# Kernel tuning notes

Hardware: AMD Instinct MI355X
Metric: run time of the kernel (lower is better)

## Reference

```python
import jax, jax.numpy as jnp
import numpy as np

EPS = 1e-5

def _act_quant(x):
    # per-token int8 absmax quantization with STE passthrough
    s = 127.0 / jnp.clip(jnp.max(jnp.abs(x), axis=-1, keepdims=True), EPS, None)
    xq = jnp.clip(jnp.round(x * s), -128.0, 127.0) / s
    return x + jax.lax.stop_gradient(xq - x)

def _weight_quant(w):
    # ternary {-1,0,1} abs-mean quantization with STE passthrough
    s = 1.0 / jnp.clip(jnp.mean(jnp.abs(w)), EPS, None)
    wq = jnp.clip(jnp.round(w * s), -1.0, 1.0) / s
    return w + jax.lax.stop_gradient(wq - w)

def bitlinear(x, w, b=None):
    y = _act_quant(x) @ _weight_quant(w).T
    return y if b is None else y + b

def setup_inputs() -> dict:
    key = jax.random.key(0)
    ks = jax.random.split(key, 6)
    B, T, C = 64, 256, 1024
    std = 1.0 / np.sqrt(C)
    return {
        "x": jax.random.normal(ks[0], (B, T, C), dtype=jnp.float32),
        "Wq": jax.random.normal(ks[1], (C, C), dtype=jnp.float32) * std,
        "Wk": jax.random.normal(ks[2], (C, C), dtype=jnp.float32) * std,
        "Wv": jax.random.normal(ks[3], (C, C), dtype=jnp.float32) * std,
        "Wp": jax.random.normal(ks[4], (C, C), dtype=jnp.float32) * std,
        "bp": jnp.zeros((C,), dtype=jnp.float32),
        "n_head": 16,
    }

def reference(x, Wq, Wk, Wv, Wp, bp, n_head):
    B, T, C = x.shape
    hd = C // n_head
    def heads(t):  # [B,T,C] -> [B,H,T,hd]
        return t.reshape(B, T, n_head, hd).transpose(0, 2, 1, 3)
    q = heads(bitlinear(x, Wq))
    k = heads(bitlinear(x, Wk))
    v = heads(bitlinear(x, Wv))
    attn = jnp.einsum("bhqd,bhkd->bhqk", q, k) * (1.0 / np.sqrt(hd))
    causal = jnp.tril(jnp.ones((T, T), dtype=bool))
    attn = jnp.where(causal, attn, -jnp.inf)
    attn = jax.nn.softmax(attn, axis=-1)
    y = jnp.einsum("bhqk,bhkd->bhqd", attn, v)
    y = y.transpose(0, 2, 1, 3).reshape(B, T, C)
    return bitlinear(y, Wp, bp)
```

## Files before the change

### kernel.cpp

```cpp
#include <hip/hip_runtime.h>
#include <math.h>

#define AS1 __attribute__((address_space(1)))
#define AS3 __attribute__((address_space(3)))

typedef unsigned short u16;
typedef signed char i8;
typedef short bf16x8 __attribute__((ext_vector_type(8)));
typedef float f32x4 __attribute__((ext_vector_type(4)));
typedef int i32x4 __attribute__((ext_vector_type(4)));

static constexpr int BB = 64, T = 256, C = 1024, H = 16, HD = 64;
static constexpr int M = BB * T;
static constexpr float EPSF = 1e-5f;

static constexpr size_t W8_OFF   = 0;
static constexpr size_t XQ8_OFF  = 4ull  << 20;
static constexpr size_t RSX_OFF  = 20ull << 20;
static constexpr size_t RSY_OFF  = (20ull << 20) + (64 << 10);
static constexpr size_t WSUM_OFF = (20ull << 20) + (128 << 10);
static constexpr size_t WPART_OFF= WSUM_OFF + 64;
static constexpr size_t QB_OFF   = 21ull << 20;
static constexpr size_t KB_OFF   = 53ull << 20;
static constexpr size_t VT_OFF   = 85ull << 20;

__device__ __forceinline__ u16 f2bf_rne(float f) {
    unsigned x = __float_as_uint(f);
    unsigned r = x + 0x7FFF + ((x >> 16) & 1);
    return (u16)(r >> 16);
}

__global__ __launch_bounds__(256) void wsum1_kernel(const float* __restrict__ Wq,
    const float* __restrict__ Wk, const float* __restrict__ Wv,
    const float* __restrict__ Wp, double* __restrict__ wpart)
{
    const int mat = blockIdx.x >> 6;
    const float* W = (mat == 0) ? Wq : (mat == 1) ? Wk : (mat == 2) ? Wv : Wp;
    const int t = threadIdx.x;
    const int base = (blockIdx.x & 63) * 256 + t;
    double s = 0.0;
    for (int i = 0; i < 64; ++i) s += (double)fabsf(W[base + (i << 14)]);
    #pragma unroll
    for (int off = 32; off >= 1; off >>= 1) s += __shfl_down(s, off);
    __shared__ double red[4];
    if ((t & 63) == 0) red[t >> 6] = s;
    __syncthreads();
    if (t == 0) wpart[blockIdx.x] = red[0] + red[1] + red[2] + red[3];
}

__global__ __launch_bounds__(256) void wsum2_kernel(const double* __restrict__ wpart,
                                                    double* __restrict__ wsum)
{
    const int t = threadIdx.x;
    double s = wpart[t];
    #pragma unroll
    for (int off = 32; off >= 1; off >>= 1) s += __shfl_down(s, off);
    if ((t & 63) == 0) wsum[t >> 6] = s;
}

__global__ __launch_bounds__(256) void wquant_kernel(const float* __restrict__ Wq,
    const float* __restrict__ Wk, const float* __restrict__ Wv,
    const float* __restrict__ Wp, const double* __restrict__ wsum,
    i8* __restrict__ w8)
{
    const int mat = blockIdx.x >> 10;
    const float* W = (mat == 0) ? Wq : (mat == 1) ? Wk : (mat == 2) ? Wv : Wp;
    const float mean = (float)(wsum[mat] * (1.0 / 1048576.0));
    const float s = 1.0f / fmaxf(mean, EPSF);
    const int idx = (blockIdx.x & 1023) * 256 + threadIdx.x;
    float4 w = ((const float4*)W)[idx];
    char4 o;
    o.x = (i8)(int)fminf(fmaxf(rintf(w.x * s), -1.f), 1.f);
    o.y = (i8)(int)fminf(fmaxf(rintf(w.y * s), -1.f), 1.f);
    o.z = (i8)(int)fminf(fmaxf(rintf(w.z * s), -1.f), 1.f);
    o.w = (i8)(int)fminf(fmaxf(rintf(w.w * s), -1.f), 1.f);
    ((char4*)(w8 + (size_t)mat * 1048576))[idx] = o;
}

__global__ __launch_bounds__(256) void actquant_kernel(const float* __restrict__ x,
    i8* __restrict__ xq, float* __restrict__ rs)
{
    const int row = blockIdx.x;
    const int t = threadIdx.x;
    float4 v = ((const float4*)(x + (size_t)row * C))[t];
    float m = fmaxf(fmaxf(fabsf(v.x), fabsf(v.y)), fmaxf(fabsf(v.z), fabsf(v.w)));
    #pragma unroll
    for (int off = 32; off >= 1; off >>= 1) m = fmaxf(m, __shfl_down(m, off));
    __shared__ float red[4];
    if ((t & 63) == 0) red[t >> 6] = m;
    __syncthreads();
    float mm = fmaxf(fmaxf(red[0], red[1]), fmaxf(red[2], red[3]));
    mm = fmaxf(mm, EPSF);
    const float s = 127.0f / mm;
    if (t == 0) rs[row] = mm / 127.0f;
    char4 o;
    o.x = (i8)(int)fminf(fmaxf(rintf(v.x * s), -128.f), 127.f);
    o.y = (i8)(int)fminf(fmaxf(rintf(v.y * s), -128.f), 127.f);
    o.z = (i8)(int)fminf(fmaxf(rintf(v.z * s), -128.f), 127.f);
    o.w = (i8)(int)fminf(fmaxf(rintf(v.w * s), -128.f), 127.f);
    ((char4*)(xq + (size_t)row * C))[t] = o;
}

template<bool QKV, int NNB>
__global__ __launch_bounds__(512, 2) void gemm_kernel(const i8* __restrict__ A,
    const i8* __restrict__ w8, const float* __restrict__ rs_row,
    const double* __restrict__ wsum, u16* __restrict__ qb, u16* __restrict__ kb,
    u16* __restrict__ vt, float* __restrict__ outp, const float* __restrict__ bias)
{
    constexpr int K = 1024, N = 1024;
    constexpr int NT = 16;
    __shared__ __align__(16) i8 Asm[4][256 * 64];
    __shared__ __align__(16) i8 Bsm[4][256 * 64];

    const int t = threadIdx.x;

    const int nwg = NNB * 64;
    const int wg = (int)blockIdx.x;
    const int swz = (wg & 7) * (nwg >> 3) + (wg >> 3);
    const int mb = swz / NNB, nb = swz % NNB;
    const int m0 = mb * 256;
    const int mat = QKV ? (nb >> 2) : 3;
    const int n0m = QKV ? ((nb & 3) * 256) : (nb * 256);
    const i8* Bw = w8 + (size_t)mat * 1048576;

    const int lane = t & 63, wv = t >> 6;
    const int wm = wv >> 2, wn = wv & 3;
    const int mr = lane & 15, quad = lane >> 4;

    const int g1 = t, g2 = t + 512;
    const int L1 = (g1 * 16) ^ (((g1 >> 3) & 7) << 4);
    const int L2 = (g2 * 16) ^ (((g2 >> 3) & 7) << 4);
    const i8* a1 = A  + (size_t)(m0  + (L1 >> 6)) * K + (L1 & 63);
    const i8* a2 = A  + (size_t)(m0  + (L2 >> 6)) * K + (L2 & 63);
    const i8* b1 = Bw + (size_t)(n0m + (L1 >> 6)) * K + (L1 & 63);
    const i8* b2 = Bw + (size_t)(n0m + (L2 >> 6)) * K + (L2 & 63);

    const int vvs = (mr >> 1) & 7;
    int aoff[8], boff[4];
    #pragma unroll
    for (int m = 0; m < 8; ++m)
        aoff[m] = ((wm * 128 + m * 16 + mr) * 64 + quad * 16) ^ (vvs << 4);
    #pragma unroll
    for (int n = 0; n < 4; ++n)
        boff[n] = ((wn * 64 + n * 16 + mr) * 64 + quad * 16) ^ (vvs << 4);

    i32x4 acc[8][4];
    #pragma unroll
    for (int m = 0; m < 8; ++m)
        #pragma unroll
        for (int n = 0; n < 4; ++n) acc[m][n] = (i32x4){0, 0, 0, 0};

    #pragma unroll
    for (int p = 0; p < 2; ++p) {
        const int k0 = p * 64;
        __builtin_amdgcn_global_load_lds((const AS1 void*)(a1 + k0), (AS3 void*)&Asm[p][g1 * 16], 16, 0, 0);
        __builtin_amdgcn_global_load_lds((const AS1 void*)(a2 + k0), (AS3 void*)&Asm[p][g2 * 16], 16, 0, 0);
        __builtin_amdgcn_global_load_lds((const AS1 void*)(b1 + k0), (AS3 void*)&Bsm[p][g1 * 16], 16, 0, 0);
        __builtin_amdgcn_global_load_lds((const AS1 void*)(b2 + k0), (AS3 void*)&Bsm[p][g2 * 16], 16, 0, 0);
    }
    asm volatile("s_waitcnt vmcnt(4)" ::: "memory");
    __builtin_amdgcn_s_barrier();

    for (int tt = 0; tt < NT; ++tt) {
        const i8* Ac = Asm[tt & 3];
        const i8* Bc = Bsm[tt & 3];
        i8* An = Asm[(tt + 2) & 3];
        i8* Bn = Bsm[(tt + 2) & 3];
        const int kn = (tt + 2) * 64;
        const bool pf = (tt < NT - 2);

        if (pf) {
            __builtin_amdgcn_global_load_lds((const AS1 void*)(a1 + kn), (AS3 void*)&An[g1 * 16], 16, 0, 0);
            __builtin_amdgcn_global_load_lds((const AS1 void*)(a2 + kn), (AS3 void*)&An[g2 * 16], 16, 0, 0);
        }
        i32x4 af[8];
        #pragma unroll
        for (int m = 0; m < 8; ++m) af[m] = *(const i32x4*)&Ac[aoff[m]];
        i32x4 bf0 = *(const i32x4*)&Bc[boff[0]];
        i32x4 bf1 = *(const i32x4*)&Bc[boff[1]];
        __builtin_amdgcn_s_barrier();
        asm volatile("s_waitcnt lgkmcnt(0)" ::: "memory");
        __builtin_amdgcn_s_setprio(1);
        #pragma unroll
        for (int m = 0; m < 8; ++m) {
            acc[m][0] = __builtin_amdgcn_mfma_i32_16x16x64_i8(af[m], bf0, acc[m][0], 0, 0, 0);
            acc[m][1] = __builtin_amdgcn_mfma_i32_16x16x64_i8(af[m], bf1, acc[m][1], 0, 0, 0);
        }
        __builtin_amdgcn_s_setprio(0);
        __builtin_amdgcn_s_barrier();

        if (pf) {
            __builtin_amdgcn_global_load_lds((const AS1 void*)(b1 + kn), (AS3 void*)&Bn[g1 * 16], 16, 0, 0);
            __builtin_amdgcn_global_load_lds((const AS1 void*)(b2 + kn), (AS3 void*)&Bn[g2 * 16], 16, 0, 0);
        }
        i32x4 bf2 = *(const i32x4*)&Bc[boff[2]];
        i32x4 bf3 = *(const i32x4*)&Bc[boff[3]];
        __builtin_amdgcn_s_barrier();
        asm volatile("s_waitcnt lgkmcnt(0)" ::: "memory");
        __builtin_amdgcn_s_setprio(1);
        #pragma unroll
        for (int m = 0; m < 8; ++m) {
            acc[m][2] = __builtin_amdgcn_mfma_i32_16x16x64_i8(af[m], bf2, acc[m][2], 0, 0, 0);
            acc[m][3] = __builtin_amdgcn_mfma_i32_16x16x64_i8(af[m], bf3, acc[m][3], 0, 0, 0);
        }
        __builtin_amdgcn_s_setprio(0);
        if (tt < NT - 2) {
            asm volatile("s_waitcnt vmcnt(4)" ::: "memory");
        } else if (tt < NT - 1) {
            asm volatile("s_waitcnt vmcnt(0)" ::: "memory");
        }
        __builtin_amdgcn_s_barrier();
    }

    float wsc = fmaxf((float)(wsum[mat] * (1.0 / 1048576.0)), EPSF);
    if (QKV && mat == 0) wsc *= 0.125f;

    if (QKV && mat == 2) {
        #pragma unroll
        for (int m = 0; m < 8; ++m) {
            const int gr0 = m0 + wm * 128 + m * 16 + quad * 4;
            const int bbi = gr0 >> 8, tl = gr0 & 255;
            const float4 rs4 = *(const float4*)(rs_row + gr0);
            #pragma unroll
            for (int n = 0; n < 4; ++n) {
                const int gcol = n0m + wn * 64 + n * 16 + mr;
                ushort4 o;
                o.x = f2bf_rne((float)acc[m][n][0] * rs4.x * wsc);
                o.y = f2bf_rne((float)acc[m][n][1] * rs4.y * wsc);
                o.z = f2bf_rne((float)acc[m][n][2] * rs4.z * wsc);
                o.w = f2bf_rne((float)acc[m][n][3] * rs4.w * wsc);
                *(ushort4*)(vt + (size_t)(bbi * 1024 + gcol) * 256 + tl) = o;
            }
        }
        return;
    }

    u16* ob = QKV ? ((mat == 0) ? qb : kb) : nullptr;
    #pragma unroll
    for (int m = 0; m < 8; ++m) {
        const int gr0 = m0 + wm * 128 + m * 16 + quad * 4;
        #pragma unroll
        for (int r = 0; r < 4; ++r) {
            const int grow = gr0 + r;
            const float sc = rs_row[grow] * wsc;
            #pragma unroll
            for (int n = 0; n < 4; ++n) {
                const int gcol = n0m + wn * 64 + n * 16 + mr;
                const float val = (float)acc[m][n][r] * sc;
                if (QKV) {
                    ob[(size_t)grow * N + gcol] = f2bf_rne(val);
                } else {
                    outp[(size_t)grow * N + gcol] = val + bias[gcol];
                }
            }
        }
    }
}

__global__ __launch_bounds__(256) void attn_kernel(const u16* __restrict__ qb,
    const u16* __restrict__ kb, const u16* __restrict__ vt, float* __restrict__ y)
{
    const int t = threadIdx.x;
    const int qt = 3 - (int)(blockIdx.x >> 10);
    const int bh = blockIdx.x & 1023;
    const int b = bh >> 4, h = bh & 15;
    const int w = t >> 6, lane = t & 63;
    const int cl = lane & 15, quad = lane >> 4;
    const size_t gb = (size_t)(b * T) * 1024 + h * 64;
    const u16* vtb = vt + (size_t)(b * 1024 + h * 64) * 256;

    const int qrow = qt * 64 + w * 16;
    const int jtiles = (qrow >> 4) + 1;

    const u16* qrp = qb + gb + (size_t)(qrow + cl) * 1024 + quad * 8;
    bf16x8 qf0 = *(const bf16x8*)qrp;
    bf16x8 qf1 = *(const bf16x8*)(qrp + 32);

    f32x4 Sp[16];
    #pragma unroll
    for (int i = 0; i < 16; ++i) Sp[i] = (f32x4){0.f, 0.f, 0.f, 0.f};

    const u16* krp = kb + gb + (size_t)cl * 1024 + quad * 8;
    #pragma unroll
    for (int jt = 0; jt < 16; ++jt) {
        if (jt < jtiles) {
            const u16* kp = krp + (size_t)(jt * 16) * 1024;
            bf16x8 kf0 = *(const bf16x8*)kp;
            bf16x8 kf1 = *(const bf16x8*)(kp + 32);
            Sp[jt] = __builtin_amdgcn_mfma_f32_16x16x32_bf16(kf0, qf0, Sp[jt], 0, 0, 0);
            Sp[jt] = __builtin_amdgcn_mfma_f32_16x16x32_bf16(kf1, qf1, Sp[jt], 0, 0, 0);
            if (jt == jtiles - 1) {
                #pragma unroll
                for (int r = 0; r < 4; ++r)
                    if (quad * 4 + r > cl) Sp[jt][r] = -INFINITY;
            }
        }
    }

    float mx = -INFINITY;
    #pragma unroll
    for (int jt = 0; jt < 16; ++jt) if (jt < jtiles) {
        #pragma unroll
        for (int r = 0; r < 4; ++r) mx = fmaxf(mx, Sp[jt][r]);
    }
    mx = fmaxf(mx, __shfl_xor(mx, 16));
    mx = fmaxf(mx, __shfl_xor(mx, 32));
    float l = 0.f;
    #pragma unroll
    for (int jt = 0; jt < 16; ++jt) if (jt < jtiles) {
        #pragma unroll
        for (int r = 0; r < 4; ++r) {
            float p = __expf(Sp[jt][r] - mx);
            Sp[jt][r] = p;
            l += p;
        }
    }
    l += __shfl_xor(l, 16);
    l += __shfl_xor(l, 32);

    f32x4 O[4];
    #pragma unroll
    for (int i = 0; i < 4; ++i) O[i] = (f32x4){0.f, 0.f, 0.f, 0.f};

    const int s01 = ((quad & 1) << 5) + cl;
    const bool lo = quad < 2;
    #pragma unroll
    for (int jc = 0; jc < 8; ++jc) {
        if (jc * 2 < jtiles) {
            int pk[2][2];
            #pragma unroll
            for (int s = 0; s < 2; ++s) {
                const f32x4 v = Sp[jc * 2 + s];
                pk[s][0] = (int)((unsigned)f2bf_rne(v[0]) | ((unsigned)f2bf_rne(v[1]) << 16));
                pk[s][1] = (int)((unsigned)f2bf_rne(v[2]) | ((unsigned)f2bf_rne(v[3]) << 16));
            }
            int a0 = __shfl(pk[0][0], s01),      a1 = __shfl(pk[0][1], s01);
            int a2 = __shfl(pk[0][0], s01 + 16), a3 = __shfl(pk[0][1], s01 + 16);
            int b0 = __shfl(pk[1][0], s01),      b1 = __shfl(pk[1][1], s01);
            int b2 = __shfl(pk[1][0], s01 + 16), b3 = __shfl(pk[1][1], s01 + 16);
            union { int i[4]; bf16x8 v; } af;
            af.i[0] = lo ? a0 : b0;
            af.i[1] = lo ? a1 : b1;
            af.i[2] = lo ? a2 : b2;
            af.i[3] = lo ? a3 : b3;
            const u16* vp = vtb + (size_t)cl * 256 + jc * 32 + quad * 8;
            #pragma unroll
            for (int dt = 0; dt < 4; ++dt) {
                bf16x8 vf = *(const bf16x8*)(vp + (size_t)dt * 16 * 256);
                O[dt] = __builtin_amdgcn_mfma_f32_16x16x32_bf16(af.v, vf, O[dt], 0, 0, 0);
            }
        }
    }

    float inv[4];
    #pragma unroll
    for (int r = 0; r < 4; ++r) inv[r] = 1.0f / __shfl(l, quad * 4 + r);
    #pragma unroll
    for (int dt = 0; dt < 4; ++dt)
        #pragma unroll
        for (int r = 0; r < 4; ++r)
            y[gb + (size_t)(qrow + quad * 4 + r) * 1024 + dt * 16 + cl] = O[dt][r] * inv[r];
}

extern "C" void kernel_launch(void* const* d_in, const int* in_sizes, int n_in,
                              void* d_out, int out_size, void* d_ws, size_t ws_size,
                              hipStream_t stream) {
    (void)in_sizes; (void)n_in; (void)out_size; (void)ws_size;
    const float* x  = (const float*)d_in[0];
    const float* Wq = (const float*)d_in[1];
    const float* Wk = (const float*)d_in[2];
    const float* Wv = (const float*)d_in[3];
    const float* Wp = (const float*)d_in[4];
    const float* bp = (const float*)d_in[5];
    float* out = (float*)d_out;
    char* ws = (char*)d_ws;

    i8*     w8   = (i8*)(ws + W8_OFF);
    i8*     xq8  = (i8*)(ws + XQ8_OFF);
    float*  rsx  = (float*)(ws + RSX_OFF);
    float*  rsy  = (float*)(ws + RSY_OFF);
    double* wsum = (double*)(ws + WSUM_OFF);
    double* wpart= (double*)(ws + WPART_OFF);
    u16*    qb   = (u16*)(ws + QB_OFF);
    u16*    kb   = (u16*)(ws + KB_OFF);
    u16*    vt   = (u16*)(ws + VT_OFF);

    wsum1_kernel<<<256, 256, 0, stream>>>(Wq, Wk, Wv, Wp, wpart);
    wsum2_kernel<<<1, 256, 0, stream>>>(wpart, wsum);
    wquant_kernel<<<4096, 256, 0, stream>>>(Wq, Wk, Wv, Wp, wsum, w8);
    actquant_kernel<<<M, 256, 0, stream>>>(x, xq8, rsx);

    gemm_kernel<true, 12><<<768, 512, 0, stream>>>(xq8, w8, rsx, wsum, qb, kb, vt, nullptr, nullptr);

    attn_kernel<<<4 * 1024, 256, 0, stream>>>(qb, kb, vt, out);

    actquant_kernel<<<M, 256, 0, stream>>>(out, xq8, rsy);
    gemm_kernel<false, 4><<<256, 512, 0, stream>>>(xq8, w8, rsy, wsum, nullptr, nullptr, nullptr, out, bp);
}
```

Measured before the change: 322.0 us.

## Merge GEMM main-loop halves into single barrier phase; remap attention block order

The int8 GEMM main loop now issues all four prefetch loads at the top of each iteration and loads every A and B fragment at once. It then runs all 32 MFMAs in one burst, so three of the four barriers and explicit lgkmcnt waits per k-step are gone, and sched_barrier fences keep the compiler from moving code across the loop boundary. The attention kernel gets a launch-bounds occupancy hint of 8 blocks and a new blockIdx mapping that interleaves the four query tiles of each group of 8 (batch,head) pairs, aiming for better K/V cache locality and load balance. Removing the mid-iteration barrier relies on the four-buffer ring and the remaining waits still keeping the LDS hazards safe. Holding all fragments live at once also raises register pressure.

```diff
diff --git a/kernel.cpp b/kernel.cpp
--- a/kernel.cpp
+++ b/kernel.cpp
@@ -160,6 +160,7 @@
     }
     asm volatile("s_waitcnt vmcnt(4)" ::: "memory");
     __builtin_amdgcn_s_barrier();
+    __builtin_amdgcn_sched_barrier(0);
 
     for (int tt = 0; tt < NT; ++tt) {
         const i8* Ac = Asm[tt & 3];
@@ -167,49 +168,35 @@
         i8* An = Asm[(tt + 2) & 3];
         i8* Bn = Bsm[(tt + 2) & 3];
         const int kn = (tt + 2) * 64;
-        const bool pf = (tt < NT - 2);
-
-        if (pf) {
+
+        if (tt < NT - 2) {
             __builtin_amdgcn_global_load_lds((const AS1 void*)(a1 + kn), (AS3 void*)&An[g1 * 16], 16, 0, 0);
             __builtin_amdgcn_global_load_lds((const AS1 void*)(a2 + kn), (AS3 void*)&An[g2 * 16], 16, 0, 0);
-        }
-        i32x4 af[8];
-        #pragma unroll
-        for (int m = 0; m < 8; ++m) af[m] = *(const i32x4*)&Ac[aoff[m]];
-        i32x4 bf0 = *(const i32x4*)&Bc[boff[0]];
-        i32x4 bf1 = *(const i32x4*)&Bc[boff[1]];
-        __builtin_amdgcn_s_barrier();
-        asm volatile("s_waitcnt lgkmcnt(0)" ::: "memory");
-        __builtin_amdgcn_s_setprio(1);
-        #pragma unroll
-        for (int m = 0; m < 8; ++m) {
-            acc[m][0] = __builtin_amdgcn_mfma_i32_16x16x64_i8(af[m], bf0, acc[m][0], 0, 0, 0);
-            acc[m][1] = __builtin_amdgcn_mfma_i32_16x16x64_i8(af[m], bf1, acc[m][1], 0, 0, 0);
-        }
-        __builtin_amdgcn_s_setprio(0);
-        __builtin_amdgcn_s_barrier();
-
-        if (pf) {
             __builtin_amdgcn_global_load_lds((const AS1 void*)(b1 + kn), (AS3 void*)&Bn[g1 * 16], 16, 0, 0);
             __builtin_amdgcn_global_load_lds((const AS1 void*)(b2 + kn), (AS3 void*)&Bn[g2 * 16], 16, 0, 0);
         }
-        i32x4 bf2 = *(const i32x4*)&Bc[boff[2]];
-        i32x4 bf3 = *(const i32x4*)&Bc[boff[3]];
-        __builtin_amdgcn_s_barrier();
-        asm volatile("s_waitcnt lgkmcnt(0)" ::: "memory");
+
+        i32x4 af[8], bf[4];
+        #pragma unroll
+        for (int m = 0; m < 8; ++m) af[m] = *(const i32x4*)&Ac[aoff[m]];
+        #pragma unroll
+        for (int n = 0; n < 4; ++n) bf[n] = *(const i32x4*)&Bc[boff[n]];
+
         __builtin_amdgcn_s_setprio(1);
         #pragma unroll
-        for (int m = 0; m < 8; ++m) {
-            acc[m][2] = __builtin_amdgcn_mfma_i32_16x16x64_i8(af[m], bf2, acc[m][2], 0, 0, 0);
-            acc[m][3] = __builtin_amdgcn_mfma_i32_16x16x64_i8(af[m], bf3, acc[m][3], 0, 0, 0);
-        }
+        for (int m = 0; m < 8; ++m)
+            #pragma unroll
+            for (int n = 0; n < 4; ++n)
+                acc[m][n] = __builtin_amdgcn_mfma_i32_16x16x64_i8(af[m], bf[n], acc[m][n], 0, 0, 0);
         __builtin_amdgcn_s_setprio(0);
+
         if (tt < NT - 2) {
             asm volatile("s_waitcnt vmcnt(4)" ::: "memory");
         } else if (tt < NT - 1) {
             asm volatile("s_waitcnt vmcnt(0)" ::: "memory");
         }
         __builtin_amdgcn_s_barrier();
+        __builtin_amdgcn_sched_barrier(0);
     }
 
     float wsc = fmaxf((float)(wsum[mat] * (1.0 / 1048576.0)), EPSF);
@@ -257,12 +244,13 @@
     }
 }
 
-__global__ __launch_bounds__(256) void attn_kernel(const u16* __restrict__ qb,
+__global__ __launch_bounds__(256, 8) void attn_kernel(const u16* __restrict__ qb,
     const u16* __restrict__ kb, const u16* __restrict__ vt, float* __restrict__ y)
 {
     const int t = threadIdx.x;
-    const int qt = 3 - (int)(blockIdx.x >> 10);
-    const int bh = blockIdx.x & 1023;
+    const int i = (int)blockIdx.x;
+    const int qt = 3 - ((i >> 3) & 3);
+    const int bh = ((i >> 5) << 3) | (i & 7);
     const int b = bh >> 4, h = bh & 15;
     const int w = t >> 6, lane = t & 63;
     const int cl = lane & 15, quad = lane >> 4;
@@ -278,7 +266,7 @@
 
     f32x4 Sp[16];
     #pragma unroll
-    for (int i = 0; i < 16; ++i) Sp[i] = (f32x4){0.f, 0.f, 0.f, 0.f};
+    for (int i2 = 0; i2 < 16; ++i2) Sp[i2] = (f32x4){0.f, 0.f, 0.f, 0.f};
 
     const u16* krp = kb + gb + (size_t)cl * 1024 + quad * 8;
     #pragma unroll
@@ -320,7 +308,7 @@
 
     f32x4 O[4];
     #pragma unroll
-    for (int i = 0; i < 4; ++i) O[i] = (f32x4){0.f, 0.f, 0.f, 0.f};
+    for (int i2 = 0; i2 < 4; ++i2) O[i2] = (f32x4){0.f, 0.f, 0.f, 0.f};
 
     const int s01 = ((quad & 1) << 5) + cl;
     const bool lo = quad < 2;
```

Measured after the change: 428.0 us. +32.9%, slower.
